# Kernel optimization log

Hardware: AMD Instinct MI355X
Metric: run time of the kernel (lower is better)

The kernel has to match this reference:

```python
import jax, jax.numpy as jnp
import numpy as np

H = 512  # hidden_dim


def setup_inputs() -> dict:
    key = jax.random.key(0)
    k1, k2, k3 = jax.random.split(key, 3)
    context = jax.random.normal(k1, (32, 512, H), dtype=jnp.float32)
    query = jax.random.normal(k2, (32, 64, H), dtype=jnp.float32)
    # similarity_linear.weight has shape (1, 3H); store flattened as (3H,)
    W = jax.random.normal(k3, (3 * H,), dtype=jnp.float32) * (1.0 / np.sqrt(3 * H))
    return {"context": context, "query": query, "W": W}


def reference(context, query, W):
    # Decompose W into the three blocks applied to [c, q, c*q].
    w_c, w_q, w_m = W[:H], W[H:2 * H], W[2 * H:]
    # S[b,i,j] = c_i.w_c + q_j.w_q + sum_d c_id * q_jd * w_m_d  -- same math as
    # Linear(3H,1) over cat([c_exp, q_exp, c_exp*q_exp]), without the O(B*C*Q*3H) tensor.
    s_c = context @ w_c                       # [B, C]
    s_q = query @ w_q                         # [B, Q]
    s_m = jnp.einsum('bcd,bqd->bcq', context * w_m, query)  # [B, C, Q]
    S = s_m + s_c[:, :, None] + s_q[:, None, :]              # [B, C, Q]

    a = jax.nn.softmax(S, axis=2)             # context-to-query attention
    attended_query = jnp.einsum('bcq,bqd->bcd', a, query)    # [B, C, H]

    b = jax.nn.softmax(jnp.max(S, axis=2), axis=1)           # [B, C]
    attended_context = jnp.einsum('bc,bcd->bd', b, context)  # [B, H]
    attended_context = jnp.broadcast_to(attended_context[:, None, :], context.shape)

    G = jnp.concatenate([
        context,
        attended_query,
        context * attended_query,
        context * attended_context,
    ], axis=2)  # [B, C, 4H]
    return G
```

## Files before the change

### kernel.cpp

```cpp
#include <hip/hip_runtime.h>
#include <cstdint>

#define NB 32
#define NC 512
#define NQ 64
#define ND 512

typedef __attribute__((ext_vector_type(8))) short bf16x8;
typedef __attribute__((ext_vector_type(4))) float f32x4;

#define PITCH 72
#define P_OFF 0
#define CM_OFF 4608
#define QQ_OFF 9216
#define QT_OFF 4608
#define AQ_F32 4608
#define AQP 68
#define SCS_F 8960
#define SQS_F 9024
#define SM_SHORTS 18176

__device__ __forceinline__ short f2bf(float f) {
  union { float f; unsigned u; } v; v.f = f;
  v.u += 0x7fffu + ((v.u >> 16) & 1u);
  return (short)(v.u >> 16);
}

__global__ __launch_bounds__(256) void k1_main(
    const float* __restrict__ ctx, const float* __restrict__ qry,
    const float* __restrict__ W, float* __restrict__ G, float* __restrict__ m_ws)
{
  __shared__ __align__(16) short sm[SM_SHORTS];
  float* smf = (float*)sm;

  const int t    = threadIdx.x;
  const int lane = t & 63;
  const int w    = t >> 6;
  const int ln15 = lane & 15;
  const int g    = lane >> 4;
  const int b    = blockIdx.x >> 3;
  const int c0   = (blockIdx.x & 7) * 64;

  const int srow = t >> 4;
  const int scol = (t & 15) * 4;

  f32x4 acc[4] = {};
  float scp[4] = {0,0,0,0}, sqp[4] = {0,0,0,0};

  for (int kc = 0; kc < 8; ++kc) {
    const int d0 = kc * 64;
    const float4 wc = *(const float4*)(W + d0 + scol);
    const float4 wq = *(const float4*)(W + ND + d0 + scol);
    const float4 wm = *(const float4*)(W + 2*ND + d0 + scol);
    __syncthreads();
    #pragma unroll
    for (int k4 = 0; k4 < 4; ++k4) {
      const int r = k4*16 + srow;
      const float4 cv = *(const float4*)(ctx + ((size_t)(b*NC + c0 + r))*ND + d0 + scol);
      const float4 qv = *(const float4*)(qry + ((size_t)(b*NQ + r))*ND + d0 + scol);
      scp[k4] += cv.x*wc.x + cv.y*wc.y + cv.z*wc.z + cv.w*wc.w;
      sqp[k4] += qv.x*wq.x + qv.y*wq.y + qv.z*wq.z + qv.w*wq.w;
      short4 cs; cs.x = f2bf(cv.x*wm.x); cs.y = f2bf(cv.y*wm.y);
                 cs.z = f2bf(cv.z*wm.z); cs.w = f2bf(cv.w*wm.w);
      short4 qs; qs.x = f2bf(qv.x); qs.y = f2bf(qv.y);
                 qs.z = f2bf(qv.z); qs.w = f2bf(qv.w);
      *(short4*)&sm[CM_OFF + r*PITCH + scol] = cs;
      *(short4*)&sm[QQ_OFF + r*PITCH + scol] = qs;
    }
    __syncthreads();
    #pragma unroll
    for (int kk = 0; kk < 2; ++kk) {
      const bf16x8 a = *(const bf16x8*)&sm[CM_OFF + (w*16 + ln15)*PITCH + kk*32 + g*8];
      #pragma unroll
      for (int n = 0; n < 4; ++n) {
        const bf16x8 bq = *(const bf16x8*)&sm[QQ_OFF + (n*16 + ln15)*PITCH + kk*32 + g*8];
        acc[n] = __builtin_amdgcn_mfma_f32_16x16x32_bf16(a, bq, acc[n], 0, 0, 0);
      }
    }
  }

  #pragma unroll
  for (int k4 = 0; k4 < 4; ++k4) {
    float v = scp[k4], u = sqp[k4];
    v += __shfl_xor(v, 1, 16); v += __shfl_xor(v, 2, 16);
    v += __shfl_xor(v, 4, 16); v += __shfl_xor(v, 8, 16);
    u += __shfl_xor(u, 1, 16); u += __shfl_xor(u, 2, 16);
    u += __shfl_xor(u, 4, 16); u += __shfl_xor(u, 8, 16);
    if (ln15 == 0) { smf[SCS_F + k4*16 + srow] = v; smf[SQS_F + k4*16 + srow] = u; }
  }
  __syncthreads();

  #pragma unroll
  for (int reg = 0; reg < 4; ++reg) {
    const int rloc = w*16 + g*4 + reg;
    const float sc = smf[SCS_F + rloc];
    float sv[4];
    #pragma unroll
    for (int n = 0; n < 4; ++n) sv[n] = acc[n][reg] + sc + smf[SQS_F + ln15 + 16*n];
    float mx = fmaxf(fmaxf(sv[0], sv[1]), fmaxf(sv[2], sv[3]));
    mx = fmaxf(mx, __shfl_xor(mx, 1, 16));
    mx = fmaxf(mx, __shfl_xor(mx, 2, 16));
    mx = fmaxf(mx, __shfl_xor(mx, 4, 16));
    mx = fmaxf(mx, __shfl_xor(mx, 8, 16));
    float s = 0.f;
    #pragma unroll
    for (int n = 0; n < 4; ++n) { sv[n] = __expf(sv[n] - mx); s += sv[n]; }
    s += __shfl_xor(s, 1, 16); s += __shfl_xor(s, 2, 16);
    s += __shfl_xor(s, 4, 16); s += __shfl_xor(s, 8, 16);
    const float inv = 1.0f / s;
    if (ln15 == 0) m_ws[b*NC + c0 + rloc] = mx;
    #pragma unroll
    for (int n = 0; n < 4; ++n)
      sm[P_OFF + rloc*PITCH + ln15 + 16*n] = f2bf(sv[n] * inv);
  }

  float* aqf = smf + AQ_F32;
  for (int dc = 0; dc < 8; ++dc) {
    const int d0 = dc * 64;
    __syncthreads();
    #pragma unroll
    for (int k4 = 0; k4 < 4; ++k4) {
      const int q = k4*16 + srow;
      const float4 qv = *(const float4*)(qry + ((size_t)(b*NQ + q))*ND + d0 + scol);
      sm[QT_OFF + (scol+0)*PITCH + (q ^ (((scol+0)>>4)*8))] = f2bf(qv.x);
      sm[QT_OFF + (scol+1)*PITCH + (q ^ (((scol+1)>>4)*8))] = f2bf(qv.y);
      sm[QT_OFF + (scol+2)*PITCH + (q ^ (((scol+2)>>4)*8))] = f2bf(qv.z);
      sm[QT_OFF + (scol+3)*PITCH + (q ^ (((scol+3)>>4)*8))] = f2bf(qv.w);
    }
    __syncthreads();
    f32x4 acc2[4] = {};
    #pragma unroll
    for (int kk = 0; kk < 2; ++kk) {
      const bf16x8 a = *(const bf16x8*)&sm[P_OFF + (w*16 + ln15)*PITCH + kk*32 + g*8];
      #pragma unroll
      for (int n = 0; n < 4; ++n) {
        const bf16x8 bq = *(const bf16x8*)&sm[QT_OFF + (n*16 + ln15)*PITCH + ((kk*32 + g*8) ^ (n*8))];
        acc2[n] = __builtin_amdgcn_mfma_f32_16x16x32_bf16(a, bq, acc2[n], 0, 0, 0);
      }
    }
    #pragma unroll
    for (int n = 0; n < 4; ++n)
      #pragma unroll
      for (int reg = 0; reg < 4; ++reg)
        aqf[(w*16 + g*4 + reg)*AQP + ln15 + 16*n] = acc2[n][reg];
    __syncthreads();
    #pragma unroll
    for (int k4 = 0; k4 < 4; ++k4) {
      const int r = k4*16 + srow;
      const float4 aq4 = *(const float4*)&aqf[r*AQP + scol];
      const float4 cv  = *(const float4*)(ctx + ((size_t)(b*NC + c0 + r))*ND + d0 + scol);
      float* gp = G + ((size_t)(b*NC + c0 + r))*2048 + d0 + scol;
      *(float4*)(gp)        = cv;
      *(float4*)(gp + 512)  = aq4;
      *(float4*)(gp + 1024) = make_float4(cv.x*aq4.x, cv.y*aq4.y,
                                          cv.z*aq4.z, cv.w*aq4.w);
    }
  }
}

__global__ __launch_bounds__(256) void k2_partial(
    const float* __restrict__ ctx, const float* __restrict__ m_ws, float* __restrict__ pc)
{
  const int t  = threadIdx.x;
  const int b  = blockIdx.x >> 4;
  const int ch = blockIdx.x & 15;
  __shared__ float r8[8];
  __shared__ float wts[32];

  const float v0 = m_ws[b*NC + t];
  const float v1 = m_ws[b*NC + 256 + t];
  float mx = fmaxf(v0, v1);
  #pragma unroll
  for (int o = 32; o; o >>= 1) mx = fmaxf(mx, __shfl_xor(mx, o, 64));
  if ((t & 63) == 0) r8[t >> 6] = mx;
  __syncthreads();
  mx = fmaxf(fmaxf(r8[0], r8[1]), fmaxf(r8[2], r8[3]));
  float e = __expf(v0 - mx) + __expf(v1 - mx);
  #pragma unroll
  for (int o = 32; o; o >>= 1) e += __shfl_xor(e, o, 64);
  if ((t & 63) == 0) r8[4 + (t >> 6)] = e;
  __syncthreads();
  const float denom = r8[4] + r8[5] + r8[6] + r8[7];
  if (t < 32) wts[t] = __expf(m_ws[b*NC + ch*32 + t] - mx) / denom;
  __syncthreads();

  float s0 = 0.f, s1 = 0.f;
  const float* base = ctx + ((size_t)(b*NC + ch*32))*ND;
  for (int c = 0; c < 32; ++c) {
    const float w = wts[c];
    s0 += w * base[(size_t)c*ND + t];
    s1 += w * base[(size_t)c*ND + t + 256];
  }
  pc[((size_t)(b*16 + ch))*ND + t]       = s0;
  pc[((size_t)(b*16 + ch))*ND + t + 256] = s1;
}

__global__ __launch_bounds__(512) void k2_reduce(
    const float* __restrict__ pc, float* __restrict__ ac)
{
  const int b = blockIdx.x;
  const int d = threadIdx.x;
  float s = 0.f;
  #pragma unroll
  for (int ch = 0; ch < 16; ++ch) s += pc[((size_t)(b*16 + ch))*ND + d];
  ac[b*ND + d] = s;
}

__global__ __launch_bounds__(256) void k3_part3(
    const float* __restrict__ ctx, const float* __restrict__ ac, float* __restrict__ G)
{
  const size_t e = ((size_t)blockIdx.x*256 + threadIdx.x) * 8;
  const int b = (int)(e >> 18);
  const int r = (int)(e & 262143);
  const int c = r >> 9;
  const int d = r & 511;
  const float4 x0 = *(const float4*)(ctx + e);
  const float4 x1 = *(const float4*)(ctx + e + 4);
  const float4 a0 = *(const float4*)(ac + b*ND + d);
  const float4 a1 = *(const float4*)(ac + b*ND + d + 4);
  float* g = G + ((size_t)(b*NC + c))*2048 + 1536 + d;
  *(float4*)(g)     = make_float4(x0.x*a0.x, x0.y*a0.y, x0.z*a0.z, x0.w*a0.w);
  *(float4*)(g + 4) = make_float4(x1.x*a1.x, x1.y*a1.y, x1.z*a1.z, x1.w*a1.w);
}

extern "C" void kernel_launch(void* const* d_in, const int* in_sizes, int n_in,
                              void* d_out, int out_size, void* d_ws, size_t ws_size,
                              hipStream_t stream)
{
  const float* ctx = (const float*)d_in[0];
  const float* qry = (const float*)d_in[1];
  const float* W   = (const float*)d_in[2];
  float* G = (float*)d_out;

  float* m_ws = (float*)d_ws;
  float* pc   = m_ws + NB*NC;
  float* ac   = pc + (size_t)NB*16*ND;

  k1_main   <<<dim3(NB*8),  dim3(256), 0, stream>>>(ctx, qry, W, G, m_ws);
  k2_partial<<<dim3(NB*16), dim3(256), 0, stream>>>(ctx, m_ws, pc);
  k2_reduce <<<dim3(NB),    dim3(512), 0, stream>>>(pc, ac);
  k3_part3  <<<dim3((NB*NC*ND)/(256*8)), dim3(256), 0, stream>>>(ctx, ac, G);
}
```

Measured before the change: 63.30 us.

## Split main kernel into score/softmax and output kernels, fuse part3 into output pass

The first kernel now only computes scores and the softmax, storing bf16 probabilities in the yet-unwritten fourth block of G as scratch and saving the row max (with the context bias moved into m_ws). A new output kernel runs after the attended-context reduction with twice as many blocks (32 context rows each). It reloads the probabilities, computes attended_query with MFMA, and writes all four G blocks in one pass, which removes the separate part3 kernel and its second read of context. The cost is an extra scratch round trip through G, a read of query in every block, and two kernels that now run serially with more dependence between them.

```diff
diff --git a/kernel.cpp b/kernel.cpp
--- a/kernel.cpp
+++ b/kernel.cpp
@@ -9,28 +9,24 @@
 typedef __attribute__((ext_vector_type(8))) short bf16x8;
 typedef __attribute__((ext_vector_type(4))) float f32x4;
 
-#define PITCH 72
-#define P_OFF 0
-#define CM_OFF 4608
-#define QQ_OFF 9216
-#define QT_OFF 4608
-#define AQ_F32 4608
-#define AQP 68
-#define SCS_F 8960
-#define SQS_F 9024
-#define SM_SHORTS 18176
-
 __device__ __forceinline__ short f2bf(float f) {
   union { float f; unsigned u; } v; v.f = f;
   v.u += 0x7fffu + ((v.u >> 16) & 1u);
   return (short)(v.u >> 16);
 }
 
-__global__ __launch_bounds__(256) void k1_main(
+#define PITCH 72
+#define CM_OFF 0
+#define QQ_OFF 4608
+#define SCS_F 4608
+#define SQS_F 4672
+#define KA_SHORTS 9472
+
+__global__ __launch_bounds__(256) void kA(
     const float* __restrict__ ctx, const float* __restrict__ qry,
     const float* __restrict__ W, float* __restrict__ G, float* __restrict__ m_ws)
 {
-  __shared__ __align__(16) short sm[SM_SHORTS];
+  __shared__ __align__(16) short sm[KA_SHORTS];
   float* smf = (float*)sm;
 
   const int t    = threadIdx.x;
@@ -93,10 +89,9 @@
   #pragma unroll
   for (int reg = 0; reg < 4; ++reg) {
     const int rloc = w*16 + g*4 + reg;
-    const float sc = smf[SCS_F + rloc];
     float sv[4];
     #pragma unroll
-    for (int n = 0; n < 4; ++n) sv[n] = acc[n][reg] + sc + smf[SQS_F + ln15 + 16*n];
+    for (int n = 0; n < 4; ++n) sv[n] = acc[n][reg] + smf[SQS_F + ln15 + 16*n];
     float mx = fmaxf(fmaxf(sv[0], sv[1]), fmaxf(sv[2], sv[3]));
     mx = fmaxf(mx, __shfl_xor(mx, 1, 16));
     mx = fmaxf(mx, __shfl_xor(mx, 2, 16));
@@ -108,44 +103,131 @@
     s += __shfl_xor(s, 1, 16); s += __shfl_xor(s, 2, 16);
     s += __shfl_xor(s, 4, 16); s += __shfl_xor(s, 8, 16);
     const float inv = 1.0f / s;
-    if (ln15 == 0) m_ws[b*NC + c0 + rloc] = mx;
-    #pragma unroll
-    for (int n = 0; n < 4; ++n)
-      sm[P_OFF + rloc*PITCH + ln15 + 16*n] = f2bf(sv[n] * inv);
-  }
-
-  float* aqf = smf + AQ_F32;
+    if (ln15 == 0) m_ws[b*NC + c0 + rloc] = mx + smf[SCS_F + rloc];
+    short* pg = (short*)(G + ((size_t)(b*NC + c0 + rloc))*2048 + 1536);
+    #pragma unroll
+    for (int n = 0; n < 4; ++n) pg[ln15 + 16*n] = f2bf(sv[n] * inv);
+  }
+}
+
+__global__ __launch_bounds__(256) void k2_partial(
+    const float* __restrict__ ctx, const float* __restrict__ m_ws, float* __restrict__ pc)
+{
+  const int t  = threadIdx.x;
+  const int b  = blockIdx.x >> 4;
+  const int ch = blockIdx.x & 15;
+  __shared__ float r8[8];
+  __shared__ float wts[32];
+
+  const float v0 = m_ws[b*NC + t];
+  const float v1 = m_ws[b*NC + 256 + t];
+  float mx = fmaxf(v0, v1);
+  #pragma unroll
+  for (int o = 32; o; o >>= 1) mx = fmaxf(mx, __shfl_xor(mx, o, 64));
+  if ((t & 63) == 0) r8[t >> 6] = mx;
+  __syncthreads();
+  mx = fmaxf(fmaxf(r8[0], r8[1]), fmaxf(r8[2], r8[3]));
+  float e = __expf(v0 - mx) + __expf(v1 - mx);
+  #pragma unroll
+  for (int o = 32; o; o >>= 1) e += __shfl_xor(e, o, 64);
+  if ((t & 63) == 0) r8[4 + (t >> 6)] = e;
+  __syncthreads();
+  const float denom = r8[4] + r8[5] + r8[6] + r8[7];
+  if (t < 32) wts[t] = __expf(m_ws[b*NC + ch*32 + t] - mx) / denom;
+  __syncthreads();
+
+  float s0 = 0.f, s1 = 0.f;
+  const float* base = ctx + ((size_t)(b*NC + ch*32))*ND;
+  for (int c = 0; c < 32; ++c) {
+    const float w = wts[c];
+    s0 += w * base[(size_t)c*ND + t];
+    s1 += w * base[(size_t)c*ND + t + 256];
+  }
+  pc[((size_t)(b*16 + ch))*ND + t]       = s0;
+  pc[((size_t)(b*16 + ch))*ND + t + 256] = s1;
+}
+
+__global__ __launch_bounds__(512) void k2_reduce(
+    const float* __restrict__ pc, float* __restrict__ ac)
+{
+  const int b = blockIdx.x;
+  const int d = threadIdx.x;
+  float s = 0.f;
+  #pragma unroll
+  for (int ch = 0; ch < 16; ++ch) s += pc[((size_t)(b*16 + ch))*ND + d];
+  ac[b*ND + d] = s;
+}
+
+#define QT_PITCH 72
+#define KB_QT_SHORTS 4608
+#define AQP 68
+__device__ __forceinline__ int qsw(int dd) {
+  return (((dd & 7) ^ ((dd >> 3) & 7)) * 8);
+}
+
+__global__ __launch_bounds__(256) void kB(
+    const float* __restrict__ ctx, const float* __restrict__ qry,
+    const float* __restrict__ ac, float* __restrict__ G)
+{
+  __shared__ __align__(16) short qt[KB_QT_SHORTS];
+  __shared__ __align__(16) float aqf[32*AQP];
+
+  const int t    = threadIdx.x;
+  const int lane = t & 63;
+  const int w    = t >> 6;
+  const int ln15 = lane & 15;
+  const int g    = lane >> 4;
+  const int cg   = w & 1;
+  const int dh   = (w >> 1) & 1;
+  const int b    = blockIdx.x >> 4;
+  const int c0   = (blockIdx.x & 15) * 32;
+
+  const int lq  = t >> 2;
+  const int ld0 = (t & 3) * 16;
+  const int srow = t >> 4;
+  const int scol = (t & 15) * 4;
+
+  bf16x8 pa[2];
+  {
+    const short* ps = (const short*)(G + ((size_t)(b*NC + c0 + cg*16 + ln15))*2048 + 1536);
+    pa[0] = *(const bf16x8*)(ps + g*8);
+    pa[1] = *(const bf16x8*)(ps + 32 + g*8);
+  }
+
   for (int dc = 0; dc < 8; ++dc) {
     const int d0 = dc * 64;
-    __syncthreads();
-    #pragma unroll
-    for (int k4 = 0; k4 < 4; ++k4) {
-      const int q = k4*16 + srow;
-      const float4 qv = *(const float4*)(qry + ((size_t)(b*NQ + q))*ND + d0 + scol);
-      sm[QT_OFF + (scol+0)*PITCH + (q ^ (((scol+0)>>4)*8))] = f2bf(qv.x);
-      sm[QT_OFF + (scol+1)*PITCH + (q ^ (((scol+1)>>4)*8))] = f2bf(qv.y);
-      sm[QT_OFF + (scol+2)*PITCH + (q ^ (((scol+2)>>4)*8))] = f2bf(qv.z);
-      sm[QT_OFF + (scol+3)*PITCH + (q ^ (((scol+3)>>4)*8))] = f2bf(qv.w);
-    }
-    __syncthreads();
-    f32x4 acc2[4] = {};
+    const float* qrow = qry + ((size_t)(b*NQ + lq))*ND + d0 + ld0;
+    #pragma unroll
+    for (int v = 0; v < 4; ++v) {
+      const float4 qv = *(const float4*)(qrow + v*4);
+      const int dd = ld0 + v*4;
+      qt[(dd+0)*QT_PITCH + (lq ^ qsw(dd+0))] = f2bf(qv.x);
+      qt[(dd+1)*QT_PITCH + (lq ^ qsw(dd+1))] = f2bf(qv.y);
+      qt[(dd+2)*QT_PITCH + (lq ^ qsw(dd+2))] = f2bf(qv.z);
+      qt[(dd+3)*QT_PITCH + (lq ^ qsw(dd+3))] = f2bf(qv.w);
+    }
+    __syncthreads();
+
+    f32x4 acc2[2] = {};
     #pragma unroll
     for (int kk = 0; kk < 2; ++kk) {
-      const bf16x8 a = *(const bf16x8*)&sm[P_OFF + (w*16 + ln15)*PITCH + kk*32 + g*8];
       #pragma unroll
-      for (int n = 0; n < 4; ++n) {
-        const bf16x8 bq = *(const bf16x8*)&sm[QT_OFF + (n*16 + ln15)*PITCH + ((kk*32 + g*8) ^ (n*8))];
-        acc2[n] = __builtin_amdgcn_mfma_f32_16x16x32_bf16(a, bq, acc2[n], 0, 0, 0);
+      for (int n = 0; n < 2; ++n) {
+        const int dd = dh*32 + n*16 + ln15;
+        const bf16x8 bq = *(const bf16x8*)&qt[dd*QT_PITCH + ((kk*32 + g*8) ^ qsw(dd))];
+        acc2[n] = __builtin_amdgcn_mfma_f32_16x16x32_bf16(pa[kk], bq, acc2[n], 0, 0, 0);
       }
     }
     #pragma unroll
-    for (int n = 0; n < 4; ++n)
+    for (int n = 0; n < 2; ++n)
       #pragma unroll
       for (int reg = 0; reg < 4; ++reg)
-        aqf[(w*16 + g*4 + reg)*AQP + ln15 + 16*n] = acc2[n][reg];
-    __syncthreads();
-    #pragma unroll
-    for (int k4 = 0; k4 < 4; ++k4) {
+        aqf[(cg*16 + g*4 + reg)*AQP + dh*32 + n*16 + ln15] = acc2[n][reg];
+    __syncthreads();
+
+    const float4 acv = *(const float4*)(ac + b*ND + d0 + scol);
+    #pragma unroll
+    for (int k4 = 0; k4 < 2; ++k4) {
       const int r = k4*16 + srow;
       const float4 aq4 = *(const float4*)&aqf[r*AQP + scol];
       const float4 cv  = *(const float4*)(ctx + ((size_t)(b*NC + c0 + r))*ND + d0 + scol);
@@ -154,73 +236,11 @@
       *(float4*)(gp + 512)  = aq4;
       *(float4*)(gp + 1024) = make_float4(cv.x*aq4.x, cv.y*aq4.y,
                                           cv.z*aq4.z, cv.w*aq4.w);
-    }
-  }
-}
-
-__global__ __launch_bounds__(256) void k2_partial(
-    const float* __restrict__ ctx, const float* __restrict__ m_ws, float* __restrict__ pc)
-{
-  const int t  = threadIdx.x;
-  const int b  = blockIdx.x >> 4;
-  const int ch = blockIdx.x & 15;
-  __shared__ float r8[8];
-  __shared__ float wts[32];
-
-  const float v0 = m_ws[b*NC + t];
-  const float v1 = m_ws[b*NC + 256 + t];
-  float mx = fmaxf(v0, v1);
-  #pragma unroll
-  for (int o = 32; o; o >>= 1) mx = fmaxf(mx, __shfl_xor(mx, o, 64));
-  if ((t & 63) == 0) r8[t >> 6] = mx;
-  __syncthreads();
-  mx = fmaxf(fmaxf(r8[0], r8[1]), fmaxf(r8[2], r8[3]));
-  float e = __expf(v0 - mx) + __expf(v1 - mx);
-  #pragma unroll
-  for (int o = 32; o; o >>= 1) e += __shfl_xor(e, o, 64);
-  if ((t & 63) == 0) r8[4 + (t >> 6)] = e;
-  __syncthreads();
-  const float denom = r8[4] + r8[5] + r8[6] + r8[7];
-  if (t < 32) wts[t] = __expf(m_ws[b*NC + ch*32 + t] - mx) / denom;
-  __syncthreads();
-
-  float s0 = 0.f, s1 = 0.f;
-  const float* base = ctx + ((size_t)(b*NC + ch*32))*ND;
-  for (int c = 0; c < 32; ++c) {
-    const float w = wts[c];
-    s0 += w * base[(size_t)c*ND + t];
-    s1 += w * base[(size_t)c*ND + t + 256];
-  }
-  pc[((size_t)(b*16 + ch))*ND + t]       = s0;
-  pc[((size_t)(b*16 + ch))*ND + t + 256] = s1;
-}
-
-__global__ __launch_bounds__(512) void k2_reduce(
-    const float* __restrict__ pc, float* __restrict__ ac)
-{
-  const int b = blockIdx.x;
-  const int d = threadIdx.x;
-  float s = 0.f;
-  #pragma unroll
-  for (int ch = 0; ch < 16; ++ch) s += pc[((size_t)(b*16 + ch))*ND + d];
-  ac[b*ND + d] = s;
-}
-
-__global__ __launch_bounds__(256) void k3_part3(
-    const float* __restrict__ ctx, const float* __restrict__ ac, float* __restrict__ G)
-{
-  const size_t e = ((size_t)blockIdx.x*256 + threadIdx.x) * 8;
-  const int b = (int)(e >> 18);
-  const int r = (int)(e & 262143);
-  const int c = r >> 9;
-  const int d = r & 511;
-  const float4 x0 = *(const float4*)(ctx + e);
-  const float4 x1 = *(const float4*)(ctx + e + 4);
-  const float4 a0 = *(const float4*)(ac + b*ND + d);
-  const float4 a1 = *(const float4*)(ac + b*ND + d + 4);
-  float* g = G + ((size_t)(b*NC + c))*2048 + 1536 + d;
-  *(float4*)(g)     = make_float4(x0.x*a0.x, x0.y*a0.y, x0.z*a0.z, x0.w*a0.w);
-  *(float4*)(g + 4) = make_float4(x1.x*a1.x, x1.y*a1.y, x1.z*a1.z, x1.w*a1.w);
+      *(float4*)(gp + 1536) = make_float4(cv.x*acv.x, cv.y*acv.y,
+                                          cv.z*acv.z, cv.w*acv.w);
+    }
+    __syncthreads();
+  }
 }
 
 extern "C" void kernel_launch(void* const* d_in, const int* in_sizes, int n_in,
@@ -236,8 +256,8 @@
   float* pc   = m_ws + NB*NC;
   float* ac   = pc + (size_t)NB*16*ND;
 
-  k1_main   <<<dim3(NB*8),  dim3(256), 0, stream>>>(ctx, qry, W, G, m_ws);
+  kA        <<<dim3(NB*8),  dim3(256), 0, stream>>>(ctx, qry, W, G, m_ws);
   k2_partial<<<dim3(NB*16), dim3(256), 0, stream>>>(ctx, m_ws, pc);
   k2_reduce <<<dim3(NB),    dim3(512), 0, stream>>>(pc, ac);
-  k3_part3  <<<dim3((NB*NC*ND)/(256*8)), dim3(256), 0, stream>>>(ctx, ac, G);
-}
+  kB        <<<dim3(NB*16), dim3(256), 0, stream>>>(ctx, qry, ac, G);
+}
```

Result: slower. 75.79 us (+19.7%).

## Move context and product writes of G into final elementwise kernel

Applied to the files above, without the earlier changes.

The main kernel now writes only the attended-query slice of G, straight from MFMA accumulators, and skips staging through shared memory and reloading context. The final kernel rereads the attended query from G and writes the context, context*attended_query and context*attended_context slices in one pass. The P operand fragments are hoisted into registers, and the q transpose uses a new XOR swizzle that reuses the CM region, which shrinks shared memory. The row-constant s_c term is dropped from the softmax and added only to the stored row max. The split adds an extra read of the attended-query slice from global memory and uses scattered scalar stores in the main kernel, in exchange for fewer shared-memory round trips and syncs.

```diff
diff --git a/kernel.cpp b/kernel.cpp
--- a/kernel.cpp
+++ b/kernel.cpp
@@ -9,24 +9,25 @@
 typedef __attribute__((ext_vector_type(8))) short bf16x8;
 typedef __attribute__((ext_vector_type(4))) float f32x4;
 
-#define PITCH 72
-#define P_OFF 0
-#define CM_OFF 4608
-#define QQ_OFF 9216
-#define QT_OFF 4608
-#define AQ_F32 4608
-#define AQP 68
-#define SCS_F 8960
-#define SQS_F 9024
-#define SM_SHORTS 18176
-
 __device__ __forceinline__ short f2bf(float f) {
   union { float f; unsigned u; } v; v.f = f;
   v.u += 0x7fffu + ((v.u >> 16) & 1u);
   return (short)(v.u >> 16);
 }
 
-__global__ __launch_bounds__(256) void k1_main(
+#define PITCH 72
+#define P_OFF  0
+#define CM_OFF 4608
+#define QQ_OFF 9216
+#define SCS_F  6912
+#define SQS_F  6976
+#define SM_SHORTS 14080
+
+__device__ __forceinline__ int qswz(int dd) {
+  return (((dd & 7) ^ ((dd >> 3) & 7)) * 8);
+}
+
+__global__ __launch_bounds__(256) void kA(
     const float* __restrict__ ctx, const float* __restrict__ qry,
     const float* __restrict__ W, float* __restrict__ G, float* __restrict__ m_ws)
 {
@@ -93,10 +94,9 @@
   #pragma unroll
   for (int reg = 0; reg < 4; ++reg) {
     const int rloc = w*16 + g*4 + reg;
-    const float sc = smf[SCS_F + rloc];
     float sv[4];
     #pragma unroll
-    for (int n = 0; n < 4; ++n) sv[n] = acc[n][reg] + sc + smf[SQS_F + ln15 + 16*n];
+    for (int n = 0; n < 4; ++n) sv[n] = acc[n][reg] + smf[SQS_F + ln15 + 16*n];
     float mx = fmaxf(fmaxf(sv[0], sv[1]), fmaxf(sv[2], sv[3]));
     mx = fmaxf(mx, __shfl_xor(mx, 1, 16));
     mx = fmaxf(mx, __shfl_xor(mx, 2, 16));
@@ -108,52 +108,52 @@
     s += __shfl_xor(s, 1, 16); s += __shfl_xor(s, 2, 16);
     s += __shfl_xor(s, 4, 16); s += __shfl_xor(s, 8, 16);
     const float inv = 1.0f / s;
-    if (ln15 == 0) m_ws[b*NC + c0 + rloc] = mx;
+    if (ln15 == 0) m_ws[b*NC + c0 + rloc] = mx + smf[SCS_F + rloc];
     #pragma unroll
     for (int n = 0; n < 4; ++n)
       sm[P_OFF + rloc*PITCH + ln15 + 16*n] = f2bf(sv[n] * inv);
   }
-
-  float* aqf = smf + AQ_F32;
+  __syncthreads();
+
+  bf16x8 pa[2];
+  #pragma unroll
+  for (int kk = 0; kk < 2; ++kk)
+    pa[kk] = *(const bf16x8*)&sm[P_OFF + (w*16 + ln15)*PITCH + kk*32 + g*8];
+
+  const int lq  = t >> 2;
+  const int ld0 = (t & 3) * 16;
+
   for (int dc = 0; dc < 8; ++dc) {
     const int d0 = dc * 64;
     __syncthreads();
-    #pragma unroll
-    for (int k4 = 0; k4 < 4; ++k4) {
-      const int q = k4*16 + srow;
-      const float4 qv = *(const float4*)(qry + ((size_t)(b*NQ + q))*ND + d0 + scol);
-      sm[QT_OFF + (scol+0)*PITCH + (q ^ (((scol+0)>>4)*8))] = f2bf(qv.x);
-      sm[QT_OFF + (scol+1)*PITCH + (q ^ (((scol+1)>>4)*8))] = f2bf(qv.y);
-      sm[QT_OFF + (scol+2)*PITCH + (q ^ (((scol+2)>>4)*8))] = f2bf(qv.z);
-      sm[QT_OFF + (scol+3)*PITCH + (q ^ (((scol+3)>>4)*8))] = f2bf(qv.w);
+    {
+      const float* qrow = qry + ((size_t)(b*NQ + lq))*ND + d0 + ld0;
+      #pragma unroll
+      for (int v = 0; v < 4; ++v) {
+        const float4 qv = *(const float4*)(qrow + v*4);
+        const int dd = ld0 + v*4;
+        sm[CM_OFF + (dd+0)*PITCH + (lq ^ qswz(dd+0))] = f2bf(qv.x);
+        sm[CM_OFF + (dd+1)*PITCH + (lq ^ qswz(dd+1))] = f2bf(qv.y);
+        sm[CM_OFF + (dd+2)*PITCH + (lq ^ qswz(dd+2))] = f2bf(qv.z);
+        sm[CM_OFF + (dd+3)*PITCH + (lq ^ qswz(dd+3))] = f2bf(qv.w);
+      }
     }
     __syncthreads();
     f32x4 acc2[4] = {};
     #pragma unroll
-    for (int kk = 0; kk < 2; ++kk) {
-      const bf16x8 a = *(const bf16x8*)&sm[P_OFF + (w*16 + ln15)*PITCH + kk*32 + g*8];
+    for (int kk = 0; kk < 2; ++kk)
       #pragma unroll
       for (int n = 0; n < 4; ++n) {
-        const bf16x8 bq = *(const bf16x8*)&sm[QT_OFF + (n*16 + ln15)*PITCH + ((kk*32 + g*8) ^ (n*8))];
-        acc2[n] = __builtin_amdgcn_mfma_f32_16x16x32_bf16(a, bq, acc2[n], 0, 0, 0);
+        const int dd = n*16 + ln15;
+        const bf16x8 bq = *(const bf16x8*)&sm[CM_OFF + dd*PITCH + ((kk*32 + g*8) ^ qswz(dd))];
+        acc2[n] = __builtin_amdgcn_mfma_f32_16x16x32_bf16(pa[kk], bq, acc2[n], 0, 0, 0);
       }
-    }
-    #pragma unroll
-    for (int n = 0; n < 4; ++n)
-      #pragma unroll
-      for (int reg = 0; reg < 4; ++reg)
-        aqf[(w*16 + g*4 + reg)*AQP + ln15 + 16*n] = acc2[n][reg];
-    __syncthreads();
-    #pragma unroll
-    for (int k4 = 0; k4 < 4; ++k4) {
-      const int r = k4*16 + srow;
-      const float4 aq4 = *(const float4*)&aqf[r*AQP + scol];
-      const float4 cv  = *(const float4*)(ctx + ((size_t)(b*NC + c0 + r))*ND + d0 + scol);
-      float* gp = G + ((size_t)(b*NC + c0 + r))*2048 + d0 + scol;
-      *(float4*)(gp)        = cv;
-      *(float4*)(gp + 512)  = aq4;
-      *(float4*)(gp + 1024) = make_float4(cv.x*aq4.x, cv.y*aq4.y,
-                                          cv.z*aq4.z, cv.w*aq4.w);
+    #pragma unroll
+    for (int reg = 0; reg < 4; ++reg) {
+      float* grow = G + ((size_t)(b*NC + c0 + w*16 + g*4 + reg))*2048 + 512 + d0;
+      #pragma unroll
+      for (int n = 0; n < 4; ++n)
+        grow[n*16 + ln15] = acc2[n][reg];
     }
   }
 }
@@ -206,7 +206,7 @@
   ac[b*ND + d] = s;
 }
 
-__global__ __launch_bounds__(256) void k3_part3(
+__global__ __launch_bounds__(256) void kFinal(
     const float* __restrict__ ctx, const float* __restrict__ ac, float* __restrict__ G)
 {
   const size_t e = ((size_t)blockIdx.x*256 + threadIdx.x) * 8;
@@ -214,13 +214,19 @@
   const int r = (int)(e & 262143);
   const int c = r >> 9;
   const int d = r & 511;
+  float* gp = G + ((size_t)(b*NC + c))*2048 + d;
   const float4 x0 = *(const float4*)(ctx + e);
   const float4 x1 = *(const float4*)(ctx + e + 4);
+  const float4 q0 = *(const float4*)(gp + 512);
+  const float4 q1 = *(const float4*)(gp + 512 + 4);
   const float4 a0 = *(const float4*)(ac + b*ND + d);
   const float4 a1 = *(const float4*)(ac + b*ND + d + 4);
-  float* g = G + ((size_t)(b*NC + c))*2048 + 1536 + d;
-  *(float4*)(g)     = make_float4(x0.x*a0.x, x0.y*a0.y, x0.z*a0.z, x0.w*a0.w);
-  *(float4*)(g + 4) = make_float4(x1.x*a1.x, x1.y*a1.y, x1.z*a1.z, x1.w*a1.w);
+  *(float4*)(gp)            = x0;
+  *(float4*)(gp + 4)        = x1;
+  *(float4*)(gp + 1024)     = make_float4(x0.x*q0.x, x0.y*q0.y, x0.z*q0.z, x0.w*q0.w);
+  *(float4*)(gp + 1024 + 4) = make_float4(x1.x*q1.x, x1.y*q1.y, x1.z*q1.z, x1.w*q1.w);
+  *(float4*)(gp + 1536)     = make_float4(x0.x*a0.x, x0.y*a0.y, x0.z*a0.z, x0.w*a0.w);
+  *(float4*)(gp + 1536 + 4) = make_float4(x1.x*a1.x, x1.y*a1.y, x1.z*a1.z, x1.w*a1.w);
 }
 
 extern "C" void kernel_launch(void* const* d_in, const int* in_sizes, int n_in,
@@ -236,8 +242,8 @@
   float* pc   = m_ws + NB*NC;
   float* ac   = pc + (size_t)NB*16*ND;
 
-  k1_main   <<<dim3(NB*8),  dim3(256), 0, stream>>>(ctx, qry, W, G, m_ws);
+  kA        <<<dim3(NB*8),  dim3(256), 0, stream>>>(ctx, qry, W, G, m_ws);
   k2_partial<<<dim3(NB*16), dim3(256), 0, stream>>>(ctx, m_ws, pc);
   k2_reduce <<<dim3(NB),    dim3(512), 0, stream>>>(pc, ac);
-  k3_part3  <<<dim3((NB*NC*ND)/(256*8)), dim3(256), 0, stream>>>(ctx, ac, G);
-}
+  kFinal    <<<dim3((NB*NC*ND)/(256*8)), dim3(256), 0, stream>>>(ctx, ac, G);
+}
```

Result: slower. 79.43 us (+25.5%).

## Precompute bf16 query and transpose once, split main kernel into single-wave blocks

Applied to the files above, without the earlier changes.

Adds a prep kernel that converts each batch's query to bf16 (row-major and transposed) and computes s_q once, instead of every context block reconverting and transposing the query in shared memory. The main kernel now uses one 64-thread wave per 16 context rows (1024 blocks, batch-swizzled), reads the context directly into MFMA registers and the bf16 query operands from global memory. This drops the LDS staging and most barriers. The s_c term is added to the row max only, since it does not change the row softmax. The cost is one extra launch and a workspace round-trip for the bf16 query, plus repeated uncoalesced global reads of the query operands served from cache.

```diff
diff --git a/kernel.cpp b/kernel.cpp
--- a/kernel.cpp
+++ b/kernel.cpp
@@ -9,94 +9,109 @@
 typedef __attribute__((ext_vector_type(8))) short bf16x8;
 typedef __attribute__((ext_vector_type(4))) float f32x4;
 
-#define PITCH 72
-#define P_OFF 0
-#define CM_OFF 4608
-#define QQ_OFF 9216
-#define QT_OFF 4608
-#define AQ_F32 4608
-#define AQP 68
-#define SCS_F 8960
-#define SQS_F 9024
-#define SM_SHORTS 18176
-
 __device__ __forceinline__ short f2bf(float f) {
   union { float f; unsigned u; } v; v.f = f;
   v.u += 0x7fffu + ((v.u >> 16) & 1u);
   return (short)(v.u >> 16);
 }
 
-__global__ __launch_bounds__(256) void k1_main(
-    const float* __restrict__ ctx, const float* __restrict__ qry,
-    const float* __restrict__ W, float* __restrict__ G, float* __restrict__ m_ws)
-{
-  __shared__ __align__(16) short sm[SM_SHORTS];
-  float* smf = (float*)sm;
+__global__ __launch_bounds__(512) void kPrep(
+    const float* __restrict__ qry, const float* __restrict__ W,
+    short* __restrict__ qbf, short* __restrict__ qTbf, float* __restrict__ s_q)
+{
+  __shared__ short lq[NQ*ND];
+  const int b = blockIdx.x;
+  const int t = threadIdx.x;
+  const int r = t >> 3;
+  const int cb = (t & 7) * 64;
+  const float* qrow = qry + ((size_t)(b*NQ + r))*ND + cb;
+  float sq = 0.f;
+  #pragma unroll
+  for (int i = 0; i < 16; ++i) {
+    const float4 qv = *(const float4*)(qrow + i*4);
+    const float4 wv = *(const float4*)(W + ND + cb + i*4);
+    sq += qv.x*wv.x + qv.y*wv.y + qv.z*wv.z + qv.w*wv.w;
+    short4 s; s.x=f2bf(qv.x); s.y=f2bf(qv.y); s.z=f2bf(qv.z); s.w=f2bf(qv.w);
+    *(short4*)&qbf[((size_t)(b*NQ + r))*ND + cb + i*4] = s;
+    *(short4*)&lq[r*ND + cb + i*4] = s;
+  }
+  sq += __shfl_xor(sq, 1, 8); sq += __shfl_xor(sq, 2, 8); sq += __shfl_xor(sq, 4, 8);
+  if ((t & 7) == 0) s_q[b*NQ + r] = sq;
+  __syncthreads();
+  const int d = t;
+  short* qTrow = qTbf + ((size_t)(b*ND + d))*NQ;
+  #pragma unroll
+  for (int j = 0; j < 16; ++j) {
+    short4 h;
+    h.x = lq[(j*4+0)*ND + d];
+    h.y = lq[(j*4+1)*ND + d];
+    h.z = lq[(j*4+2)*ND + d];
+    h.w = lq[(j*4+3)*ND + d];
+    *(short4*)&qTrow[j*4] = h;
+  }
+}
+
+__global__ __launch_bounds__(64) void kS(
+    const float* __restrict__ ctx, const float* __restrict__ W,
+    const short* __restrict__ qbf, const short* __restrict__ qTbf,
+    const float* __restrict__ s_q, float* __restrict__ G, float* __restrict__ m_ws)
+{
+  __shared__ __align__(16) short P[16*72];
+  __shared__ __align__(16) float aqf[16*68];
+  __shared__ float scf[16];
 
   const int t    = threadIdx.x;
-  const int lane = t & 63;
-  const int w    = t >> 6;
-  const int ln15 = lane & 15;
-  const int g    = lane >> 4;
-  const int b    = blockIdx.x >> 3;
-  const int c0   = (blockIdx.x & 7) * 64;
-
-  const int srow = t >> 4;
-  const int scol = (t & 15) * 4;
+  const int ln15 = t & 15;
+  const int g    = t >> 4;
+  const int bid  = (int)blockIdx.x;
+  const int swz  = (bid & 7) * 128 + (bid >> 3);
+  const int b    = swz >> 5;
+  const int c0   = (swz & 31) * 16;
+
+  const float* crow = ctx + ((size_t)(b*NC + c0 + ln15))*ND;
 
   f32x4 acc[4] = {};
-  float scp[4] = {0,0,0,0}, sqp[4] = {0,0,0,0};
-
+  float scp = 0.f;
+
+  #pragma unroll 2
   for (int kc = 0; kc < 8; ++kc) {
-    const int d0 = kc * 64;
-    const float4 wc = *(const float4*)(W + d0 + scol);
-    const float4 wq = *(const float4*)(W + ND + d0 + scol);
-    const float4 wm = *(const float4*)(W + 2*ND + d0 + scol);
-    __syncthreads();
-    #pragma unroll
-    for (int k4 = 0; k4 < 4; ++k4) {
-      const int r = k4*16 + srow;
-      const float4 cv = *(const float4*)(ctx + ((size_t)(b*NC + c0 + r))*ND + d0 + scol);
-      const float4 qv = *(const float4*)(qry + ((size_t)(b*NQ + r))*ND + d0 + scol);
-      scp[k4] += cv.x*wc.x + cv.y*wc.y + cv.z*wc.z + cv.w*wc.w;
-      sqp[k4] += qv.x*wq.x + qv.y*wq.y + qv.z*wq.z + qv.w*wq.w;
-      short4 cs; cs.x = f2bf(cv.x*wm.x); cs.y = f2bf(cv.y*wm.y);
-                 cs.z = f2bf(cv.z*wm.z); cs.w = f2bf(cv.w*wm.w);
-      short4 qs; qs.x = f2bf(qv.x); qs.y = f2bf(qv.y);
-                 qs.z = f2bf(qv.z); qs.w = f2bf(qv.w);
-      *(short4*)&sm[CM_OFF + r*PITCH + scol] = cs;
-      *(short4*)&sm[QQ_OFF + r*PITCH + scol] = qs;
-    }
-    __syncthreads();
     #pragma unroll
     for (int kk = 0; kk < 2; ++kk) {
-      const bf16x8 a = *(const bf16x8*)&sm[CM_OFF + (w*16 + ln15)*PITCH + kk*32 + g*8];
+      const int dd = kc*64 + kk*32 + g*8;
+      const float4 c0v = *(const float4*)(crow + dd);
+      const float4 c1v = *(const float4*)(crow + dd + 4);
+      const float4 wc0 = *(const float4*)(W + dd);
+      const float4 wc1 = *(const float4*)(W + dd + 4);
+      const float4 wm0 = *(const float4*)(W + 2*ND + dd);
+      const float4 wm1 = *(const float4*)(W + 2*ND + dd + 4);
+      scp += c0v.x*wc0.x + c0v.y*wc0.y + c0v.z*wc0.z + c0v.w*wc0.w
+           + c1v.x*wc1.x + c1v.y*wc1.y + c1v.z*wc1.z + c1v.w*wc1.w;
+      bf16x8 a;
+      a[0]=f2bf(c0v.x*wm0.x); a[1]=f2bf(c0v.y*wm0.y); a[2]=f2bf(c0v.z*wm0.z); a[3]=f2bf(c0v.w*wm0.w);
+      a[4]=f2bf(c1v.x*wm1.x); a[5]=f2bf(c1v.y*wm1.y); a[6]=f2bf(c1v.z*wm1.z); a[7]=f2bf(c1v.w*wm1.w);
       #pragma unroll
       for (int n = 0; n < 4; ++n) {
-        const bf16x8 bq = *(const bf16x8*)&sm[QQ_OFF + (n*16 + ln15)*PITCH + kk*32 + g*8];
+        const bf16x8 bq = *(const bf16x8*)&qbf[((size_t)(b*NQ + n*16 + ln15))*ND + dd];
         acc[n] = __builtin_amdgcn_mfma_f32_16x16x32_bf16(a, bq, acc[n], 0, 0, 0);
       }
     }
   }
 
-  #pragma unroll
-  for (int k4 = 0; k4 < 4; ++k4) {
-    float v = scp[k4], u = sqp[k4];
-    v += __shfl_xor(v, 1, 16); v += __shfl_xor(v, 2, 16);
-    v += __shfl_xor(v, 4, 16); v += __shfl_xor(v, 8, 16);
-    u += __shfl_xor(u, 1, 16); u += __shfl_xor(u, 2, 16);
-    u += __shfl_xor(u, 4, 16); u += __shfl_xor(u, 8, 16);
-    if (ln15 == 0) { smf[SCS_F + k4*16 + srow] = v; smf[SQS_F + k4*16 + srow] = u; }
-  }
-  __syncthreads();
+  scp += __shfl_xor(scp, 16, 64);
+  scp += __shfl_xor(scp, 32, 64);
+  if (g == 0) scf[ln15] = scp;
+  __syncthreads();
+
+  float sqv[4];
+  #pragma unroll
+  for (int n = 0; n < 4; ++n) sqv[n] = s_q[b*NQ + n*16 + ln15];
 
   #pragma unroll
   for (int reg = 0; reg < 4; ++reg) {
-    const int rloc = w*16 + g*4 + reg;
-    const float sc = smf[SCS_F + rloc];
+    const int rloc = g*4 + reg;
     float sv[4];
     #pragma unroll
-    for (int n = 0; n < 4; ++n) sv[n] = acc[n][reg] + sc + smf[SQS_F + ln15 + 16*n];
+    for (int n = 0; n < 4; ++n) sv[n] = acc[n][reg] + sqv[n];
     float mx = fmaxf(fmaxf(sv[0], sv[1]), fmaxf(sv[2], sv[3]));
     mx = fmaxf(mx, __shfl_xor(mx, 1, 16));
     mx = fmaxf(mx, __shfl_xor(mx, 2, 16));
@@ -108,48 +123,40 @@
     s += __shfl_xor(s, 1, 16); s += __shfl_xor(s, 2, 16);
     s += __shfl_xor(s, 4, 16); s += __shfl_xor(s, 8, 16);
     const float inv = 1.0f / s;
-    if (ln15 == 0) m_ws[b*NC + c0 + rloc] = mx;
+    if (ln15 == 0) m_ws[b*NC + c0 + rloc] = mx + scf[rloc];
     #pragma unroll
     for (int n = 0; n < 4; ++n)
-      sm[P_OFF + rloc*PITCH + ln15 + 16*n] = f2bf(sv[n] * inv);
-  }
-
-  float* aqf = smf + AQ_F32;
+      P[rloc*72 + ln15 + 16*n] = f2bf(sv[n] * inv);
+  }
+  __syncthreads();
+
+  bf16x8 pa[2];
+  pa[0] = *(const bf16x8*)&P[ln15*72 + g*8];
+  pa[1] = *(const bf16x8*)&P[ln15*72 + 32 + g*8];
+
   for (int dc = 0; dc < 8; ++dc) {
     const int d0 = dc * 64;
-    __syncthreads();
-    #pragma unroll
-    for (int k4 = 0; k4 < 4; ++k4) {
-      const int q = k4*16 + srow;
-      const float4 qv = *(const float4*)(qry + ((size_t)(b*NQ + q))*ND + d0 + scol);
-      sm[QT_OFF + (scol+0)*PITCH + (q ^ (((scol+0)>>4)*8))] = f2bf(qv.x);
-      sm[QT_OFF + (scol+1)*PITCH + (q ^ (((scol+1)>>4)*8))] = f2bf(qv.y);
-      sm[QT_OFF + (scol+2)*PITCH + (q ^ (((scol+2)>>4)*8))] = f2bf(qv.z);
-      sm[QT_OFF + (scol+3)*PITCH + (q ^ (((scol+3)>>4)*8))] = f2bf(qv.w);
-    }
-    __syncthreads();
     f32x4 acc2[4] = {};
     #pragma unroll
-    for (int kk = 0; kk < 2; ++kk) {
-      const bf16x8 a = *(const bf16x8*)&sm[P_OFF + (w*16 + ln15)*PITCH + kk*32 + g*8];
+    for (int kk = 0; kk < 2; ++kk)
       #pragma unroll
       for (int n = 0; n < 4; ++n) {
-        const bf16x8 bq = *(const bf16x8*)&sm[QT_OFF + (n*16 + ln15)*PITCH + ((kk*32 + g*8) ^ (n*8))];
-        acc2[n] = __builtin_amdgcn_mfma_f32_16x16x32_bf16(a, bq, acc2[n], 0, 0, 0);
+        const bf16x8 bq = *(const bf16x8*)&qTbf[((size_t)(b*ND + d0 + n*16 + ln15))*NQ + kk*32 + g*8];
+        acc2[n] = __builtin_amdgcn_mfma_f32_16x16x32_bf16(pa[kk], bq, acc2[n], 0, 0, 0);
       }
-    }
+    __syncthreads();
     #pragma unroll
     for (int n = 0; n < 4; ++n)
       #pragma unroll
       for (int reg = 0; reg < 4; ++reg)
-        aqf[(w*16 + g*4 + reg)*AQP + ln15 + 16*n] = acc2[n][reg];
+        aqf[(g*4 + reg)*68 + n*16 + ln15] = acc2[n][reg];
     __syncthreads();
     #pragma unroll
-    for (int k4 = 0; k4 < 4; ++k4) {
-      const int r = k4*16 + srow;
-      const float4 aq4 = *(const float4*)&aqf[r*AQP + scol];
-      const float4 cv  = *(const float4*)(ctx + ((size_t)(b*NC + c0 + r))*ND + d0 + scol);
-      float* gp = G + ((size_t)(b*NC + c0 + r))*2048 + d0 + scol;
+    for (int pass = 0; pass < 4; ++pass) {
+      const int r = pass*4 + g;
+      const float4 aq4 = *(const float4*)&aqf[r*68 + ln15*4];
+      const float4 cv  = *(const float4*)(ctx + ((size_t)(b*NC + c0 + r))*ND + d0 + ln15*4);
+      float* gp = G + ((size_t)(b*NC + c0 + r))*2048 + d0 + ln15*4;
       *(float4*)(gp)        = cv;
       *(float4*)(gp + 512)  = aq4;
       *(float4*)(gp + 1024) = make_float4(cv.x*aq4.x, cv.y*aq4.y,
@@ -206,7 +213,7 @@
   ac[b*ND + d] = s;
 }
 
-__global__ __launch_bounds__(256) void k3_part3(
+__global__ __launch_bounds__(256) void kFinal(
     const float* __restrict__ ctx, const float* __restrict__ ac, float* __restrict__ G)
 {
   const size_t e = ((size_t)blockIdx.x*256 + threadIdx.x) * 8;
@@ -218,9 +225,9 @@
   const float4 x1 = *(const float4*)(ctx + e + 4);
   const float4 a0 = *(const float4*)(ac + b*ND + d);
   const float4 a1 = *(const float4*)(ac + b*ND + d + 4);
-  float* g = G + ((size_t)(b*NC + c))*2048 + 1536 + d;
-  *(float4*)(g)     = make_float4(x0.x*a0.x, x0.y*a0.y, x0.z*a0.z, x0.w*a0.w);
-  *(float4*)(g + 4) = make_float4(x1.x*a1.x, x1.y*a1.y, x1.z*a1.z, x1.w*a1.w);
+  float* gp = G + ((size_t)(b*NC + c))*2048 + 1536 + d;
+  *(float4*)(gp)     = make_float4(x0.x*a0.x, x0.y*a0.y, x0.z*a0.z, x0.w*a0.w);
+  *(float4*)(gp + 4) = make_float4(x1.x*a1.x, x1.y*a1.y, x1.z*a1.z, x1.w*a1.w);
 }
 
 extern "C" void kernel_launch(void* const* d_in, const int* in_sizes, int n_in,
@@ -232,12 +239,17 @@
   const float* W   = (const float*)d_in[2];
   float* G = (float*)d_out;
 
-  float* m_ws = (float*)d_ws;
-  float* pc   = m_ws + NB*NC;
-  float* ac   = pc + (size_t)NB*16*ND;
-
-  k1_main   <<<dim3(NB*8),  dim3(256), 0, stream>>>(ctx, qry, W, G, m_ws);
+  float* ws   = (float*)d_ws;
+  float* m_ws = ws;
+  float* pc   = ws + 16384;
+  float* ac   = ws + 278528;
+  float* s_q  = ws + 294912;
+  short* qbf  = (short*)(ws + 296960);
+  short* qTbf = qbf + (size_t)NB*NQ*ND;
+
+  kPrep     <<<dim3(NB),    dim3(512), 0, stream>>>(qry, W, qbf, qTbf, s_q);
+  kS        <<<dim3(NB*32), dim3(64),  0, stream>>>(ctx, W, qbf, qTbf, s_q, G, m_ws);
   k2_partial<<<dim3(NB*16), dim3(256), 0, stream>>>(ctx, m_ws, pc);
   k2_reduce <<<dim3(NB),    dim3(512), 0, stream>>>(pc, ac);
-  k3_part3  <<<dim3((NB*NC*ND)/(256*8)), dim3(256), 0, stream>>>(ctx, ac, G);
-}
+  kFinal    <<<dim3((NB*NC*ND)/(256*8)), dim3(256), 0, stream>>>(ctx, ac, G);
+}
```

After: 77.02 us. +21.7%, slower.
